# Optimization experiments

Measured on AMD Instinct MI355X. Metric: run time of the kernel, lower is better.

Reference implementation:

```python
import jax, jax.numpy as jnp
import numpy as np
from jax import lax

N_CLASS, SOS, EOS, NEG = 5, 0, 4, -10000.0


def _lstm_dir(x, Wih, Whh, bih, bhh, reverse):
    # x: (T, B, Din); PyTorch gate order i, f, g, o
    T, B, _ = x.shape
    Hd = Whh.shape[1]
    h0 = jnp.zeros((B, Hd), x.dtype)

    def step(carry, xt):
        h, c = carry
        g = xt @ Wih.T + h @ Whh.T + bih + bhh
        i, f, gg, o = jnp.split(g, 4, axis=-1)
        c = jax.nn.sigmoid(f) * c + jax.nn.sigmoid(i) * jnp.tanh(gg)
        h = jax.nn.sigmoid(o) * jnp.tanh(c)
        return (h, c), h

    xs = x[::-1] if reverse else x
    _, hs = lax.scan(step, (h0, h0), xs)
    return hs[::-1] if reverse else hs


def _forward(input_ids, tags, mask, emb, convs, lstm_params, lin_w, lin_b, transition):
    T, B = mask.shape
    x = emb[input_ids][:, None]  # (N, 1, L, E)
    pooled = []
    for w, b in convs:  # w: (K, 1, size, E)
        c = lax.conv_general_dilated(x, w, (1, 1), 'VALID',
                                     dimension_numbers=('NCHW', 'OIHW', 'NCHW'))
        c = jax.nn.relu(c[..., 0] + b[None, :, None])  # (N, K, L-size+1)
        pooled.append(jnp.max(c, axis=2))              # max-pool over length
    para = jnp.concatenate(pooled, axis=1)             # (N, 3K)
    h = para.reshape(B, T, -1).transpose(1, 0, 2)      # (T, B, 3K); equal para_len
    for (Wf, Uf, bf, cf, Wb, Ub, bb, cb) in lstm_params:  # 2-layer BiLSTM (eval: no dropout)
        hf = _lstm_dir(h, Wf, Uf, bf, cf, False)
        hb = _lstm_dir(h, Wb, Ub, bb, cb, True)
        h = jnp.concatenate([hf, hb], axis=-1)
    m = mask[..., None]
    feats = ((h * m) @ lin_w.T + lin_b) * m            # (T, B, 5)

    # CRF forward algorithm (log partition)
    alpha0 = jnp.full((B, N_CLASS), NEG, feats.dtype).at[:, SOS].set(0.0)

    def step(alpha, inp):
        feat, mt = inp
        s = alpha[:, None, :] + transition[None] + feat[:, :, None]
        new = jax.nn.logsumexp(s, axis=-1)
        return new * mt[:, None] + alpha * (1.0 - mt[:, None]), None

    alpha, _ = lax.scan(step, alpha0, (feats, mask))
    fwd_score = jax.nn.logsumexp(alpha + transition[EOS][None], axis=-1)

    # gold path score
    tags_ext = jnp.concatenate([jnp.full((1, B), SOS, tags.dtype), tags], 0)  # (T+1, B)
    emit = jnp.take_along_axis(feats, tags[..., None], axis=-1)[..., 0]       # (T, B)
    trans = transition[tags_ext[1:], tags_ext[:-1]]                           # (T, B)
    gold = jnp.sum((emit + trans) * mask, axis=0)
    lengths = mask.sum(0).astype(jnp.int32)
    last = tags_ext[lengths, jnp.arange(B)]
    gold = gold + transition[EOS, last]
    return (fwd_score - gold).sum()


def setup_inputs() -> dict:
    key = jax.random.key(0)
    ks = jax.random.split(key, 32)
    B, T, L, V, E, K, H = 8, 64, 64, 50000, 768, 256, 64
    N = B * T
    inp = {}
    inp['input_ids'] = jax.random.randint(ks[0], (N, L), 1, V)
    inp['tags'] = jax.random.randint(ks[1], (T, B), 1, 4)  # B/I/O tags
    inp['mask'] = jnp.ones((T, B), jnp.float32)
    inp['para_len'] = jnp.full((B,), T, jnp.int32)
    inp['emb'] = jax.random.normal(ks[2], (V, E)) * 0.1
    for i, sz in enumerate((3, 4, 5)):
        inp[f'cw{sz}'] = jax.random.normal(ks[3 + i], (K, 1, sz, E)) * (1.0 / np.sqrt(sz * E))
        inp[f'cb{sz}'] = jnp.zeros((K,), jnp.float32)
    kidx = 6
    for layer, din in ((0, 3 * K), (1, 2 * H)):
        for d in 'fb':
            inp[f'Wih{layer}{d}'] = jax.random.normal(ks[kidx], (4 * H, din)) * (1.0 / np.sqrt(din)); kidx += 1
            inp[f'Whh{layer}{d}'] = jax.random.normal(ks[kidx], (4 * H, H)) * (1.0 / np.sqrt(H)); kidx += 1
            inp[f'bih{layer}{d}'] = jnp.zeros((4 * H,), jnp.float32)
            inp[f'bhh{layer}{d}'] = jnp.zeros((4 * H,), jnp.float32)
    inp['lin_w'] = jax.random.normal(ks[kidx], (N_CLASS, 2 * H)) * 0.1; kidx += 1
    inp['lin_b'] = jnp.zeros((N_CLASS,), jnp.float32)
    tr = jax.random.normal(ks[kidx], (N_CLASS, N_CLASS))
    inp['transition'] = tr.at[SOS, :].set(NEG).at[:, EOS].set(NEG)
    return inp


def reference(input_ids, tags, mask, para_len, emb, cw3, cb3, cw4, cb4, cw5, cb5,
              Wih0f, Whh0f, bih0f, bhh0f, Wih0b, Whh0b, bih0b, bhh0b,
              Wih1f, Whh1f, bih1f, bhh1f, Wih1b, Whh1b, bih1b, bhh1b,
              lin_w, lin_b, transition):
    convs = ((cw3, cb3), (cw4, cb4), (cw5, cb5))
    lstm_params = ((Wih0f, Whh0f, bih0f, bhh0f, Wih0b, Whh0b, bih0b, bhh0b),
                   (Wih1f, Whh1f, bih1f, bhh1f, Wih1b, Whh1b, bih1b, bhh1b))
    return _forward(input_ids, tags, mask, emb, convs, lstm_params, lin_w, lin_b, transition)
```

## Files before the change

### kernel.cpp

```cpp
#include <hip/hip_runtime.h>
#include <cstdint>
#include <cstddef>

#define DEV __device__ __forceinline__

typedef __bf16 bf16x8 __attribute__((ext_vector_type(8)));
typedef float f32x4 __attribute__((ext_vector_type(4)));

#define NEG_VAL -10000.0f

DEV unsigned int f2bf(float f) {
    unsigned int u = __float_as_uint(f);
    return (u + 0x7FFFu + ((u >> 16) & 1u)) >> 16;
}
DEV unsigned int pk2(float a, float b) { return f2bf(a) | (f2bf(b) << 16); }

DEV float sigf(float x)  { return __builtin_amdgcn_rcpf(1.f + __expf(-x)); }
DEV float tanhff(float x){ return 2.f * __builtin_amdgcn_rcpf(1.f + __expf(-2.f * x)) - 1.f; }

__global__ void cast_all_kernel(const float* __restrict__ cw3,
                                const float* __restrict__ cw4,
                                const float* __restrict__ cw5,
                                const float* __restrict__ Wih0f,
                                const float* __restrict__ Wih0b,
                                const float* __restrict__ Wih1f,
                                const float* __restrict__ Wih1b,
                                unsigned short* __restrict__ wbc,
                                unsigned short* __restrict__ wih0c,
                                unsigned short* __restrict__ wih1c) {
    int tid = blockIdx.x * blockDim.x + threadIdx.x;
    const float* src;
    uint4* dstp;
    if (tid < 294912) {
        int g   = tid & 3;
        int col = (tid >> 2) & 255;
        int c   = (tid >> 10) % 24;
        int p   = tid / (24 * 256 * 4);
        int sz, j; const float* W;
        if (p < 3)      { sz = 3; j = p;     W = cw3; }
        else if (p < 7) { sz = 4; j = p - 3; W = cw4; }
        else            { sz = 5; j = p - 7; W = cw5; }
        src = W + ((size_t)col * sz + j) * 768 + c * 32 + g * 8;
        dstp = reinterpret_cast<uint4*>(wbc) +
               ((size_t)(p * 24 + c) * 1024 + (col >> 4) * 64 + g * 16 + (col & 15));
    } else if (tid < 294912 + 49152) {
        int u   = tid - 294912;
        int g   = u & 3;
        int col = (u >> 2) & 255;
        int kc  = (u >> 10) % 24;
        int dir = u / (24 * 256 * 4);
        const float* W = dir ? Wih0b : Wih0f;
        src = W + (size_t)col * 768 + kc * 32 + g * 8;
        dstp = reinterpret_cast<uint4*>(wih0c) +
               ((size_t)(dir * 24 + kc) * 1024 + (col >> 4) * 64 + g * 16 + (col & 15));
    } else if (tid < 294912 + 49152 + 8192) {
        int u   = tid - 294912 - 49152;
        int g   = u & 3;
        int col = (u >> 2) & 255;
        int kc  = (u >> 10) % 4;
        int dir = u / (4 * 256 * 4);
        const float* W = dir ? Wih1b : Wih1f;
        src = W + (size_t)col * 128 + kc * 32 + g * 8;
        dstp = reinterpret_cast<uint4*>(wih1c) +
               ((size_t)(dir * 4 + kc) * 1024 + (col >> 4) * 64 + g * 16 + (col & 15));
    } else return;
    float4 a = *(const float4*)(src);
    float4 b = *(const float4*)(src + 4);
    *dstp = make_uint4(pk2(a.x, a.y), pk2(a.z, a.w), pk2(b.x, b.y), pk2(b.z, b.w));
}

template<int SZ>
DEV void conv_body(const int* __restrict__ ids,
                   const float* __restrict__ emb,
                   const unsigned short* __restrict__ wbc,
                   const float* __restrict__ cb,
                   unsigned short* __restrict__ para_bf,
                   int pair, int szi, int pbase,
                   unsigned short* Xlds)
{
    int tid  = threadIdx.x;
    int lane = tid & 63;
    int nw   = tid >> 6;
    int l15  = lane & 15;
    int q    = lane >> 4;
    int n0   = pair * 2;

    int srow  = tid >> 1;
    int shalf = tid & 1;
    int sid   = ids[(n0 + (srow >> 6)) * 64 + (srow & 63)];
    const float* embrow = emb + (size_t)sid * 768 + shalf * 16;
    int skey = (srow >> 1) & 3;
    int xo0 = srow * 32 + (((2 * shalf)     ^ skey) * 8);
    int xo1 = srow * 32 + (((2 * shalf + 1) ^ skey) * 8);

    int vlaneB = nw * 2048 + lane * 8;

    f32x4 acc[8][4];
    #pragma unroll
    for (int a = 0; a < 8; a++)
        #pragma unroll
        for (int t = 0; t < 4; t++) acc[a][t] = (f32x4){0.f, 0.f, 0.f, 0.f};

    bf16x8 bfr[2][4];
    float4 e0, e1, e2, e3;

    {
        e0 = ((const float4*)embrow)[0];
        e1 = ((const float4*)embrow)[1];
        e2 = ((const float4*)embrow)[2];
        e3 = ((const float4*)embrow)[3];
        const unsigned short* bt = wbc + (size_t)(pbase * 24) * 8192 + vlaneB;
        #pragma unroll
        for (int t = 0; t < 4; t++)
            bfr[0][t] = *(const bf16x8*)(bt + t * 512);
        uint4 p0 = make_uint4(pk2(e0.x, e0.y), pk2(e0.z, e0.w),
                              pk2(e1.x, e1.y), pk2(e1.z, e1.w));
        uint4 p1 = make_uint4(pk2(e2.x, e2.y), pk2(e2.z, e2.w),
                              pk2(e3.x, e3.y), pk2(e3.z, e3.w));
        *(uint4*)&Xlds[xo0] = p0;
        *(uint4*)&Xlds[xo1] = p1;
        asm volatile("s_waitcnt lgkmcnt(0)" ::: "memory");
        __builtin_amdgcn_s_barrier();
    }

    int cbase = pbase * 24;
    for (int c2 = 0; c2 < 24; c2 += 2, cbase += 2) {
        #pragma unroll
        for (int s2 = 0; s2 < 2 * SZ; ++s2) {
            const int half = (s2 < SZ) ? 0 : 1;
            const int j    = s2 - half * SZ;
            const int par  = s2 & 1;
            {
                const int sP = s2 + 1;
                const int offP = (sP < SZ) ? sP * 24
                               : (sP < 2 * SZ ? (sP - SZ) * 24 + 1 : 2);
                const unsigned short* bt =
                    wbc + (size_t)(cbase + offP) * 8192 + vlaneB;
                #pragma unroll
                for (int t = 0; t < 4; t++)
                    bfr[par ^ 1][t] = *(const bf16x8*)(bt + t * 512);
            }
            if (s2 == 0 || s2 == SZ) {
                int cE = half ? c2 + 2 : c2 + 1; if (cE > 23) cE = 0;
                const float* sp = embrow + cE * 32;
                e0 = ((const float4*)sp)[0];
                e1 = ((const float4*)sp)[1];
                e2 = ((const float4*)sp)[2];
                e3 = ((const float4*)sp)[3];
            }

            const unsigned short* Xb = Xlds + half * 4096;
            {
                bf16x8 af[4];
                #pragma unroll
                for (int a = 0; a < 4; a++) {
                    int pp = 16 * a + l15 + j; if (pp > 63) pp = 63;
                    af[a] = *(const bf16x8*)(
                        &Xb[pp * 32 + ((q ^ ((pp >> 1) & 3)) * 8)]);
                }
                __builtin_amdgcn_s_setprio(1);
                #pragma unroll
                for (int a = 0; a < 4; a++)
                    #pragma unroll
                    for (int t = 0; t < 4; t++)
                        acc[a][t] = __builtin_amdgcn_mfma_f32_16x16x32_bf16(
                            af[a], bfr[par][t], acc[a][t], 0, 0, 0);
                __builtin_amdgcn_s_setprio(0);
            }
            {
                bf16x8 af[4];
                #pragma unroll
                for (int a = 0; a < 4; a++) {
                    int pp = 16 * a + l15 + j; if (pp > 63) pp = 63;
                    int xr = 64 + pp;
                    af[a] = *(const bf16x8*)(
                        &Xb[xr * 32 + ((q ^ ((xr >> 1) & 3)) * 8)]);
                }
                __builtin_amdgcn_s_setprio(1);
                #pragma unroll
                for (int a = 0; a < 4; a++)
                    #pragma unroll
                    for (int t = 0; t < 4; t++)
                        acc[4 + a][t] = __builtin_amdgcn_mfma_f32_16x16x32_bf16(
                            af[a], bfr[par][t], acc[4 + a][t], 0, 0, 0);
                __builtin_amdgcn_s_setprio(0);
            }

            if (j == SZ - 1) {
                unsigned short* Xw = Xlds + (half ^ 1) * 4096;
                uint4 p0 = make_uint4(pk2(e0.x, e0.y), pk2(e0.z, e0.w),
                                      pk2(e1.x, e1.y), pk2(e1.z, e1.w));
                uint4 p1 = make_uint4(pk2(e2.x, e2.y), pk2(e2.z, e2.w),
                                      pk2(e3.x, e3.y), pk2(e3.z, e3.w));
                *(uint4*)&Xw[xo0] = p0;
                *(uint4*)&Xw[xo1] = p1;
                asm volatile("s_waitcnt lgkmcnt(0)" ::: "memory");
                __builtin_amdgcn_s_barrier();
            }
        }
    }

    int pmax = 64 - SZ;
    #pragma unroll
    for (int t = 0; t < 4; t++) {
        int colb = nw * 64 + t * 16;
        float bias = cb[colb + l15];
        #pragma unroll
        for (int s = 0; s < 2; s++) {
            float m = 0.0f;
            #pragma unroll
            for (int a4 = 0; a4 < 4; a4++) {
                #pragma unroll
                for (int r = 0; r < 4; r++) {
                    int p = 16 * a4 + q * 4 + r;
                    float v = acc[s * 4 + a4][t][r] + bias;
                    v = v > 0.f ? v : 0.f;
                    if (p <= pmax) m = v > m ? v : m;
                }
            }
            m = fmaxf(m, __shfl_xor(m, 16));
            m = fmaxf(m, __shfl_xor(m, 32));
            if (lane < 16) {
                int n = n0 + s;
                int row = (n & 63) * 8 + (n >> 6);
                para_bf[(size_t)row * 768 + szi * 256 + colb + lane] =
                    (unsigned short)f2bf(m);
            }
        }
    }
}

__global__ __launch_bounds__(256, 2) void conv_pool_kernel(
    const int* __restrict__ ids,
    const float* __restrict__ emb,
    const unsigned short* __restrict__ wbc,
    const float* __restrict__ cb3, const float* __restrict__ cb4,
    const float* __restrict__ cb5,
    unsigned short* __restrict__ para_bf)
{
    __shared__ unsigned short Xlds[2][4096];
    int bx   = blockIdx.x;
    int szi  = 2 - (bx >> 8);
    int pair = bx & 255;
    if (szi == 0)
        conv_body<3>(ids, emb, wbc, cb3, para_bf, pair, 0, 0, &Xlds[0][0]);
    else if (szi == 1)
        conv_body<4>(ids, emb, wbc, cb4, para_bf, pair, 1, 3, &Xlds[0][0]);
    else
        conv_body<5>(ids, emb, wbc, cb5, para_bf, pair, 2, 7, &Xlds[0][0]);
}

template<int KC>
__global__ __launch_bounds__(256) void gemm_in_kernel(
    const unsigned short* __restrict__ xbf,
    const unsigned short* __restrict__ wihc,
    const float* __restrict__ bihF, const float* __restrict__ bhhF,
    const float* __restrict__ bihB, const float* __restrict__ bhhB,
    float* __restrict__ gates2)
{
    const int din = KC * 32;
    int bx   = blockIdx.x;
    int dir  = bx >> 4;
    int rowg = (bx >> 1) & 7;
    int colg = bx & 1;
    int tid  = threadIdx.x;
    int lane = tid & 63;
    int wid  = tid >> 6;
    int mw   = wid >> 1;
    int nw   = wid & 1;
    int l15  = lane & 15;
    int q    = lane >> 4;

    const float* bih = dir ? bihB : bihF;
    const float* bhh = dir ? bhhB : bhhF;
    const unsigned short* wt = wihc + (size_t)dir * KC * 8192;

    const unsigned short* arow[2];
    #pragma unroll
    for (int a = 0; a < 2; a++)
        arow[a] = xbf + (size_t)(rowg * 64 + mw * 32 + a * 16 + l15) * din + q * 8;
    const unsigned short* bbase = wt + (colg * 8 + nw * 4) * 512 + lane * 8;

    f32x4 acc[2][4];
    #pragma unroll
    for (int a = 0; a < 2; a++)
        #pragma unroll
        for (int t = 0; t < 4; t++) acc[a][t] = (f32x4){0.f, 0.f, 0.f, 0.f};

    bf16x8 afb[4][2], bfb[4][4];
    #pragma unroll
    for (int s = 0; s < 3; s++) {
        int k0 = (s < KC) ? s : KC - 1;
        #pragma unroll
        for (int a = 0; a < 2; a++)
            afb[s][a] = *(const bf16x8*)(arow[a] + k0 * 32);
        #pragma unroll
        for (int t = 0; t < 4; t++)
            bfb[s][t] = *(const bf16x8*)(bbase + (size_t)k0 * 8192 + t * 512);
    }

    #pragma unroll 4
    for (int kc = 0; kc < KC; ++kc) {
        const int p  = kc & 3;
        const int pn = (kc + 3) & 3;
        int kn = (kc + 3 < KC) ? kc + 3 : KC - 1;
        #pragma unroll
        for (int a = 0; a < 2; a++)
            afb[pn][a] = *(const bf16x8*)(arow[a] + kn * 32);
        #pragma unroll
        for (int t = 0; t < 4; t++)
            bfb[pn][t] = *(const bf16x8*)(bbase + (size_t)kn * 8192 + t * 512);
        #pragma unroll
        for (int a = 0; a < 2; a++)
            #pragma unroll
            for (int t = 0; t < 4; t++)
                acc[a][t] = __builtin_amdgcn_mfma_f32_16x16x32_bf16(
                    afb[p][a], bfb[p][t], acc[a][t], 0, 0, 0);
    }

    #pragma unroll
    for (int tt = 0; tt < 4; tt++) {
        int nn = colg * 128 + nw * 64 + tt * 16 + l15;
        float bb = bih[nn] + bhh[nn];
        #pragma unroll
        for (int a = 0; a < 2; a++) {
            int m = rowg * 64 + mw * 32 + q * 4 + a * 16;
            int tcol = m >> 3, b0 = m & 7;
            f32x4 v = acc[a][tt];
            v[0] += bb; v[1] += bb; v[2] += bb; v[3] += bb;
            *(f32x4*)(gates2 + (((size_t)dir * 64 + tcol) * 256 + nn) * 8 + b0) = v;
        }
    }
}

__global__ __launch_bounds__(256) void lstm_rec_kernel(
    const float* __restrict__ gates2,
    const float* __restrict__ WhhF, const float* __restrict__ WhhB,
    float* __restrict__ houtF,
    unsigned short* __restrict__ houtB)
{
    int dir = blockIdx.x;
    const float* Whh = dir ? WhhB : WhhF;
    const float* gin = gates2 + (size_t)dir * 64 * 256 * 8;

    __shared__ unsigned short h16[2][16 * 64];

    int tid  = threadIdx.x;
    int lane = tid & 63;
    int w    = tid >> 6;
    int l15  = lane & 15;
    int q    = lane >> 4;
    int hh   = 16 * w + l15;

    bf16x8 Bf[4][2];
    #pragma unroll
    for (int g = 0; g < 4; g++)
        #pragma unroll
        for (int kh = 0; kh < 2; kh++) {
            const float* wp = Whh + (size_t)(g * 64 + hh) * 64 + kh * 32 + q * 8;
            float4 f0 = *(const float4*)wp;
            float4 f1 = *(const float4*)(wp + 4);
            bf16x8 r;
            r[0] = (__bf16)f0.x; r[1] = (__bf16)f0.y;
            r[2] = (__bf16)f0.z; r[3] = (__bf16)f0.w;
            r[4] = (__bf16)f1.x; r[5] = (__bf16)f1.y;
            r[6] = (__bf16)f1.z; r[7] = (__bf16)f1.w;
            Bf[g][kh] = r;
        }

    const float* pgB[4];
    #pragma unroll
    for (int g = 0; g < 4; g++)
        pgB[g] = gin + (size_t)(g * 64 + hh) * 8 + 4 * q;

    for (int i = tid; i < 2 * 16 * 64; i += 256)
        ((unsigned short*)h16)[i] = 0;
    float cst[4] = {0.f, 0.f, 0.f, 0.f};
    __syncthreads();

    f32x4 gvp[4][4];
    #pragma unroll
    for (int d = 0; d < 3; d++) {
        int td = dir ? 63 - d : d;
        #pragma unroll
        for (int g = 0; g < 4; g++)
            gvp[d][g] = *(const f32x4*)(pgB[g] + (size_t)td * 2048);
    }

    #pragma unroll 4
    for (int s = 0; s < 64; ++s) {
        const int slot = s & 3;
        int t = dir ? 63 - s : s;
        const unsigned short* hb = h16[s & 1];
        int slot0 = q ^ (l15 & 7);
        int slot1 = (4 + q) ^ (l15 & 7);
        bf16x8 a0 = *(const bf16x8*)&hb[l15 * 64 + slot0 * 8];
        bf16x8 a1 = *(const bf16x8*)&hb[l15 * 64 + slot1 * 8];

        f32x4 acc[4];
        #pragma unroll
        for (int g = 0; g < 4; g++) {
            acc[g] = __builtin_amdgcn_mfma_f32_16x16x32_bf16(a0, Bf[g][0], gvp[slot][g], 0, 0, 0);
            acc[g] = __builtin_amdgcn_mfma_f32_16x16x32_bf16(a1, Bf[g][1], acc[g], 0, 0, 0);
        }

        {
            int sn = (s + 3 < 64) ? s + 3 : 63;
            int tn = dir ? 63 - sn : sn;
            const int slotn = (s + 3) & 3;
            #pragma unroll
            for (int g = 0; g < 4; g++)
                gvp[slotn][g] = *(const f32x4*)(pgB[g] + (size_t)tn * 2048);
        }

        if (q < 2) {
            unsigned short* hw = h16[(s + 1) & 1];
            #pragma unroll
            for (int r = 0; r < 4; r++) {
                int b = 4 * q + r;
                float gi = acc[0][r];
                float gf = acc[1][r];
                float gg = acc[2][r];
                float go = acc[3][r];
                float cn = sigf(gf) * cst[r] + sigf(gi) * tanhff(gg);
                float hv = sigf(go) * tanhff(cn);
                cst[r] = cn;
                int slotw = (hh >> 3) ^ (b & 7);
                hw[b * 64 + slotw * 8 + (hh & 7)] = (unsigned short)f2bf(hv);
                size_t oi = ((size_t)t * 8 + b) * 128 + dir * 64 + hh;
                if (houtF) houtF[oi] = hv;
                houtB[oi] = (unsigned short)f2bf(hv);
            }
        }
        __syncthreads();
    }
}

__global__ __launch_bounds__(512) void crf_kernel(
    const float* __restrict__ h1,
    const float* __restrict__ lin_w,
    const float* __restrict__ lin_b,
    const float* __restrict__ mask,
    const int* __restrict__ tags,
    const float* __restrict__ trans,
    float* __restrict__ out) {
    __shared__ float feats[64][8][5];
    __shared__ float wl[5][128];
    __shared__ float msk[512];
    __shared__ int   tgs[512];
    __shared__ float fwd_s[8], gold_s[8];
    __shared__ float tr[25], trE[5], lb[5];
    int tid = threadIdx.x;
    if (tid < 25) tr[tid] = trans[tid];
    if (tid < 5) { trE[tid] = trans[20 + tid]; lb[tid] = lin_b[tid]; }
    msk[tid] = mask[tid];
    tgs[tid] = tags[tid];
    if (tid < 128) {
        #pragma unroll
        for (int i = 0; i < 5; i++) wl[i][tid] = lin_w[i * 128 + tid];
    }
    __syncthreads();

    {
        const float4* h4 = (const float4*)(h1 + (size_t)tid * 128);
        float a0 = 0.f, a1 = 0.f, a2 = 0.f, a3 = 0.f, a4 = 0.f;
        for (int e4 = 0; e4 < 32; e4++) {
            float4 hv = h4[e4];
            int e = e4 * 4;
            a0 += hv.x * wl[0][e] + hv.y * wl[0][e+1] + hv.z * wl[0][e+2] + hv.w * wl[0][e+3];
            a1 += hv.x * wl[1][e] + hv.y * wl[1][e+1] + hv.z * wl[1][e+2] + hv.w * wl[1][e+3];
            a2 += hv.x * wl[2][e] + hv.y * wl[2][e+1] + hv.z * wl[2][e+2] + hv.w * wl[2][e+3];
            a3 += hv.x * wl[3][e] + hv.y * wl[3][e+1] + hv.z * wl[3][e+2] + hv.w * wl[3][e+3];
            a4 += hv.x * wl[4][e] + hv.y * wl[4][e+1] + hv.z * wl[4][e+2] + hv.w * wl[4][e+3];
        }
        float m = msk[tid];
        int t = tid >> 3, b = tid & 7;
        feats[t][b][0] = (m * a0 + lb[0]) * m;
        feats[t][b][1] = (m * a1 + lb[1]) * m;
        feats[t][b][2] = (m * a2 + lb[2]) * m;
        feats[t][b][3] = (m * a3 + lb[3]) * m;
        feats[t][b][4] = (m * a4 + lb[4]) * m;
    }
    __syncthreads();

    if (tid < 40) {
        int b = tid / 5, i = tid % 5;
        float alpha = (i == 0) ? 0.f : NEG_VAL;
        float trow[5];
        #pragma unroll
        for (int j2 = 0; j2 < 5; j2++) trow[j2] = tr[i * 5 + j2];
        for (int t = 0; t < 64; t++) {
            float s0, s1, s2, s3, s4;
            s0 = __shfl(alpha, b * 5 + 0, 64) + trow[0];
            s1 = __shfl(alpha, b * 5 + 1, 64) + trow[1];
            s2 = __shfl(alpha, b * 5 + 2, 64) + trow[2];
            s3 = __shfl(alpha, b * 5 + 3, 64) + trow[3];
            s4 = __shfl(alpha, b * 5 + 4, 64) + trow[4];
            float mx = fmaxf(fmaxf(fmaxf(s0, s1), fmaxf(s2, s3)), s4);
            float sum = expf(s0 - mx) + expf(s1 - mx) + expf(s2 - mx) +
                        expf(s3 - mx) + expf(s4 - mx);
            float lse = mx + logf(sum) + feats[t][b][i];
            float mt = msk[t * 8 + b];
            alpha = mt * lse + (1.f - mt) * alpha;
        }
        float v = alpha + trE[i];
        float m0 = __shfl(v, b * 5 + 0, 64);
        float m1 = __shfl(v, b * 5 + 1, 64);
        float m2 = __shfl(v, b * 5 + 2, 64);
        float m3 = __shfl(v, b * 5 + 3, 64);
        float m4 = __shfl(v, b * 5 + 4, 64);
        float mx = fmaxf(fmaxf(fmaxf(m0, m1), fmaxf(m2, m3)), m4);
        float sum = expf(m0 - mx) + expf(m1 - mx) + expf(m2 - mx) +
                    expf(m3 - mx) + expf(m4 - mx);
        if (i == 0) fwd_s[b] = mx + logf(sum);
    }
    if (tid >= 64 && tid < 72) {
        int b = tid - 64;
        float g = 0.f, lenf = 0.f;
        int prev = 0;
        for (int t = 0; t < 64; t++) {
            int tg = tgs[t * 8 + b];
            float mt = msk[t * 8 + b];
            g += (feats[t][b][tg] + tr[tg * 5 + prev]) * mt;
            lenf += mt;
            prev = tg;
        }
        int len = (int)lenf;
        int last = (len == 0) ? 0 : tgs[(len - 1) * 8 + b];
        g += trE[last];
        gold_s[b] = g;
    }
    __syncthreads();
    if (tid == 0) {
        float s = 0.f;
        for (int b = 0; b < 8; b++) s += fwd_s[b] - gold_s[b];
        out[0] = s;
    }
}

extern "C" void kernel_launch(void* const* d_in, const int* in_sizes, int n_in,
                              void* d_out, int out_size, void* d_ws, size_t ws_size,
                              hipStream_t stream) {
    const int*   ids   = (const int*)d_in[0];
    const int*   tags  = (const int*)d_in[1];
    const float* mask  = (const float*)d_in[2];
    const float* emb   = (const float*)d_in[4];
    const float* cw3   = (const float*)d_in[5];
    const float* cb3   = (const float*)d_in[6];
    const float* cw4   = (const float*)d_in[7];
    const float* cb4   = (const float*)d_in[8];
    const float* cw5   = (const float*)d_in[9];
    const float* cb5   = (const float*)d_in[10];
    const float* Wih0f = (const float*)d_in[11];
    const float* Whh0f = (const float*)d_in[12];
    const float* bih0f = (const float*)d_in[13];
    const float* bhh0f = (const float*)d_in[14];
    const float* Wih0b = (const float*)d_in[15];
    const float* Whh0b = (const float*)d_in[16];
    const float* bih0b = (const float*)d_in[17];
    const float* bhh0b = (const float*)d_in[18];
    const float* Wih1f = (const float*)d_in[19];
    const float* Whh1f = (const float*)d_in[20];
    const float* bih1f = (const float*)d_in[21];
    const float* bhh1f = (const float*)d_in[22];
    const float* Wih1b = (const float*)d_in[23];
    const float* Whh1b = (const float*)d_in[24];
    const float* bih1b = (const float*)d_in[25];
    const float* bhh1b = (const float*)d_in[26];
    const float* lin_w = (const float*)d_in[27];
    const float* lin_b = (const float*)d_in[28];
    const float* trans = (const float*)d_in[29];

    char* ws = (char*)d_ws;
    unsigned short* wbc     = (unsigned short*)ws;
    unsigned short* wih0c   = (unsigned short*)(ws + 4718592);
    unsigned short* wih1c   = (unsigned short*)(ws + 5505024);
    unsigned short* para_bf = (unsigned short*)(ws + 5636096);
    float*          gates   = (float*)(ws + 6422528);
    unsigned short* h0_bf   = (unsigned short*)(ws + 5636096);
    float*          h1f     = (float*)(ws + 4718592);

    hipLaunchKernelGGL(cast_all_kernel, dim3(1376), dim3(256), 0, stream,
                       cw3, cw4, cw5, Wih0f, Wih0b, Wih1f, Wih1b,
                       wbc, wih0c, wih1c);
    hipLaunchKernelGGL(conv_pool_kernel, dim3(768), dim3(256), 0, stream,
                       ids, emb, wbc, cb3, cb4, cb5, para_bf);
    hipLaunchKernelGGL((gemm_in_kernel<24>), dim3(32), dim3(256), 0, stream,
                       para_bf, wih0c, bih0f, bhh0f, bih0b, bhh0b, gates);
    hipLaunchKernelGGL(lstm_rec_kernel, dim3(2), dim3(256), 0, stream,
                       gates, Whh0f, Whh0b, (float*)nullptr, h0_bf);
    hipLaunchKernelGGL((gemm_in_kernel<4>), dim3(32), dim3(256), 0, stream,
                       h0_bf, wih1c, bih1f, bhh1f, bih1b, bhh1b, gates);
    hipLaunchKernelGGL(lstm_rec_kernel, dim3(2), dim3(256), 0, stream,
                       gates, Whh1f, Whh1b, h1f, h0_bf);
    hipLaunchKernelGGL(crf_kernel, dim3(1), dim3(512), 0, stream,
                       h1f, lin_w, lin_b, mask, tags, trans, (float*)d_out);
}
```

Before: 250.3 us.

## Fuse GEMM, LSTM recurrence and CRF stages into one cooperative kernel

```diff
diff --git a/kernel.cpp b/kernel.cpp
--- a/kernel.cpp
+++ b/kernel.cpp
@@ -1,6 +1,9 @@
 #include <hip/hip_runtime.h>
+#include <hip/hip_cooperative_groups.h>
 #include <cstdint>
 #include <cstddef>
+
+namespace cg = cooperative_groups;
 
 #define DEV __device__ __forceinline__
 
@@ -250,16 +253,30 @@
         conv_body<5>(ids, emb, wbc, cb5, para_bf, pair, 2, 7, &Xlds[0][0]);
 }
 
+struct TailArgs {
+    const unsigned short* para_bf;
+    const unsigned short* wih0c;
+    const unsigned short* wih1c;
+    const float *bih0f, *bhh0f, *bih0b, *bhh0b;
+    const float *bih1f, *bhh1f, *bih1b, *bhh1b;
+    const float *Whh0f, *Whh0b, *Whh1f, *Whh1b;
+    float* gates;
+    unsigned short* h0_bf;
+    float* h1f;
+    const float* lin_w; const float* lin_b;
+    const float* mask; const int* tags; const float* trans;
+    float* out;
+};
+
 template<int KC>
-__global__ __launch_bounds__(256) void gemm_in_kernel(
-    const unsigned short* __restrict__ xbf,
-    const unsigned short* __restrict__ wihc,
-    const float* __restrict__ bihF, const float* __restrict__ bhhF,
-    const float* __restrict__ bihB, const float* __restrict__ bhhB,
-    float* __restrict__ gates2)
+DEV void gemm_phase(int bx,
+                    const unsigned short* __restrict__ xbf,
+                    const unsigned short* __restrict__ wihc,
+                    const float* bihF, const float* bhhF,
+                    const float* bihB, const float* bhhB,
+                    float* __restrict__ gates2)
 {
     const int din = KC * 32;
-    int bx   = blockIdx.x;
     int dir  = bx >> 4;
     int rowg = (bx >> 1) & 7;
     int colg = bx & 1;
@@ -333,17 +350,15 @@
     }
 }
 
-__global__ __launch_bounds__(256) void lstm_rec_kernel(
-    const float* __restrict__ gates2,
-    const float* __restrict__ WhhF, const float* __restrict__ WhhB,
-    float* __restrict__ houtF,
-    unsigned short* __restrict__ houtB)
+DEV void lstm_phase(char* smemraw, int dir,
+                    const float* __restrict__ gates2,
+                    const float* __restrict__ Whh,
+                    float* __restrict__ houtF,
+                    unsigned short* __restrict__ houtB)
 {
-    int dir = blockIdx.x;
-    const float* Whh = dir ? WhhB : WhhF;
+    unsigned short (*h16)[16 * 64] =
+        reinterpret_cast<unsigned short (*)[16 * 64]>(smemraw);
     const float* gin = gates2 + (size_t)dir * 64 * 256 * 8;
-
-    __shared__ unsigned short h16[2][16 * 64];
 
     int tid  = threadIdx.x;
     int lane = tid & 63;
@@ -436,50 +451,57 @@
     }
 }
 
-__global__ __launch_bounds__(512) void crf_kernel(
-    const float* __restrict__ h1,
-    const float* __restrict__ lin_w,
-    const float* __restrict__ lin_b,
-    const float* __restrict__ mask,
-    const int* __restrict__ tags,
-    const float* __restrict__ trans,
-    float* __restrict__ out) {
-    __shared__ float feats[64][8][5];
-    __shared__ float wl[5][128];
-    __shared__ float msk[512];
-    __shared__ int   tgs[512];
-    __shared__ float fwd_s[8], gold_s[8];
-    __shared__ float tr[25], trE[5], lb[5];
+struct CrfSmem {
+    float feats[64][8][5];
+    float wl[5][128];
+    float msk[512];
+    int   tgs[512];
+    float fwd_s[8], gold_s[8];
+    float tr[25], trE[5], lb[5];
+};
+
+DEV void crf_phase(char* smemraw,
+                   const float* __restrict__ h1,
+                   const float* __restrict__ lin_w,
+                   const float* __restrict__ lin_b,
+                   const float* __restrict__ mask,
+                   const int* __restrict__ tags,
+                   const float* __restrict__ trans,
+                   float* __restrict__ out)
+{
+    CrfSmem& S = *reinterpret_cast<CrfSmem*>(smemraw);
     int tid = threadIdx.x;
-    if (tid < 25) tr[tid] = trans[tid];
-    if (tid < 5) { trE[tid] = trans[20 + tid]; lb[tid] = lin_b[tid]; }
-    msk[tid] = mask[tid];
-    tgs[tid] = tags[tid];
+    if (tid < 25) S.tr[tid] = trans[tid];
+    if (tid < 5) { S.trE[tid] = trans[20 + tid]; S.lb[tid] = lin_b[tid]; }
+    for (int i = tid; i < 512; i += 256) {
+        S.msk[i] = mask[i];
+        S.tgs[i] = tags[i];
+    }
     if (tid < 128) {
         #pragma unroll
-        for (int i = 0; i < 5; i++) wl[i][tid] = lin_w[i * 128 + tid];
+        for (int i = 0; i < 5; i++) S.wl[i][tid] = lin_w[i * 128 + tid];
     }
     __syncthreads();
 
-    {
-        const float4* h4 = (const float4*)(h1 + (size_t)tid * 128);
+    for (int rr = tid; rr < 512; rr += 256) {
+        const float4* h4 = (const float4*)(h1 + (size_t)rr * 128);
         float a0 = 0.f, a1 = 0.f, a2 = 0.f, a3 = 0.f, a4 = 0.f;
         for (int e4 = 0; e4 < 32; e4++) {
             float4 hv = h4[e4];
             int e = e4 * 4;
-            a0 += hv.x * wl[0][e] + hv.y * wl[0][e+1] + hv.z * wl[0][e+2] + hv.w * wl[0][e+3];
-            a1 += hv.x * wl[1][e] + hv.y * wl[1][e+1] + hv.z * wl[1][e+2] + hv.w * wl[1][e+3];
-            a2 += hv.x * wl[2][e] + hv.y * wl[2][e+1] + hv.z * wl[2][e+2] + hv.w * wl[2][e+3];
-            a3 += hv.x * wl[3][e] + hv.y * wl[3][e+1] + hv.z * wl[3][e+2] + hv.w * wl[3][e+3];
-            a4 += hv.x * wl[4][e] + hv.y * wl[4][e+1] + hv.z * wl[4][e+2] + hv.w * wl[4][e+3];
-        }
-        float m = msk[tid];
-        int t = tid >> 3, b = tid & 7;
-        feats[t][b][0] = (m * a0 + lb[0]) * m;
-        feats[t][b][1] = (m * a1 + lb[1]) * m;
-        feats[t][b][2] = (m * a2 + lb[2]) * m;
-        feats[t][b][3] = (m * a3 + lb[3]) * m;
-        feats[t][b][4] = (m * a4 + lb[4]) * m;
+            a0 += hv.x * S.wl[0][e] + hv.y * S.wl[0][e+1] + hv.z * S.wl[0][e+2] + hv.w * S.wl[0][e+3];
+            a1 += hv.x * S.wl[1][e] + hv.y * S.wl[1][e+1] + hv.z * S.wl[1][e+2] + hv.w * S.wl[1][e+3];
+            a2 += hv.x * S.wl[2][e] + hv.y * S.wl[2][e+1] + hv.z * S.wl[2][e+2] + hv.w * S.wl[2][e+3];
+            a3 += hv.x * S.wl[3][e] + hv.y * S.wl[3][e+1] + hv.z * S.wl[3][e+2] + hv.w * S.wl[3][e+3];
+            a4 += hv.x * S.wl[4][e] + hv.y * S.wl[4][e+1] + hv.z * S.wl[4][e+2] + hv.w * S.wl[4][e+3];
+        }
+        float m = S.msk[rr];
+        int t = rr >> 3, b = rr & 7;
+        S.feats[t][b][0] = (m * a0 + S.lb[0]) * m;
+        S.feats[t][b][1] = (m * a1 + S.lb[1]) * m;
+        S.feats[t][b][2] = (m * a2 + S.lb[2]) * m;
+        S.feats[t][b][3] = (m * a3 + S.lb[3]) * m;
+        S.feats[t][b][4] = (m * a4 + S.lb[4]) * m;
     }
     __syncthreads();
 
@@ -488,7 +510,7 @@
         float alpha = (i == 0) ? 0.f : NEG_VAL;
         float trow[5];
         #pragma unroll
-        for (int j2 = 0; j2 < 5; j2++) trow[j2] = tr[i * 5 + j2];
+        for (int j2 = 0; j2 < 5; j2++) trow[j2] = S.tr[i * 5 + j2];
         for (int t = 0; t < 64; t++) {
             float s0, s1, s2, s3, s4;
             s0 = __shfl(alpha, b * 5 + 0, 64) + trow[0];
@@ -499,11 +521,11 @@
             float mx = fmaxf(fmaxf(fmaxf(s0, s1), fmaxf(s2, s3)), s4);
             float sum = expf(s0 - mx) + expf(s1 - mx) + expf(s2 - mx) +
                         expf(s3 - mx) + expf(s4 - mx);
-            float lse = mx + logf(sum) + feats[t][b][i];
-            float mt = msk[t * 8 + b];
+            float lse = mx + logf(sum) + S.feats[t][b][i];
+            float mt = S.msk[t * 8 + b];
             alpha = mt * lse + (1.f - mt) * alpha;
         }
-        float v = alpha + trE[i];
+        float v = alpha + S.trE[i];
         float m0 = __shfl(v, b * 5 + 0, 64);
         float m1 = __shfl(v, b * 5 + 1, 64);
         float m2 = __shfl(v, b * 5 + 2, 64);
@@ -512,30 +534,55 @@
         float mx = fmaxf(fmaxf(fmaxf(m0, m1), fmaxf(m2, m3)), m4);
         float sum = expf(m0 - mx) + expf(m1 - mx) + expf(m2 - mx) +
                     expf(m3 - mx) + expf(m4 - mx);
-        if (i == 0) fwd_s[b] = mx + logf(sum);
+        if (i == 0) S.fwd_s[b] = mx + logf(sum);
     }
     if (tid >= 64 && tid < 72) {
         int b = tid - 64;
         float g = 0.f, lenf = 0.f;
         int prev = 0;
         for (int t = 0; t < 64; t++) {
-            int tg = tgs[t * 8 + b];
-            float mt = msk[t * 8 + b];
-            g += (feats[t][b][tg] + tr[tg * 5 + prev]) * mt;
+            int tg = S.tgs[t * 8 + b];
+            float mt = S.msk[t * 8 + b];
+            g += (S.feats[t][b][tg] + S.tr[tg * 5 + prev]) * mt;
             lenf += mt;
             prev = tg;
         }
         int len = (int)lenf;
-        int last = (len == 0) ? 0 : tgs[(len - 1) * 8 + b];
-        g += trE[last];
-        gold_s[b] = g;
+        int last = (len == 0) ? 0 : S.tgs[(len - 1) * 8 + b];
+        g += S.trE[last];
+        S.gold_s[b] = g;
     }
     __syncthreads();
     if (tid == 0) {
         float s = 0.f;
-        for (int b = 0; b < 8; b++) s += fwd_s[b] - gold_s[b];
+        for (int b = 0; b < 8; b++) s += S.fwd_s[b] - S.gold_s[b];
         out[0] = s;
     }
+}
+
+__global__ __launch_bounds__(256) void tail_kernel(TailArgs a)
+{
+    cg::grid_group grid = cg::this_grid();
+    __shared__ __align__(16) char smem[sizeof(CrfSmem)];
+    int bx = blockIdx.x;
+
+    gemm_phase<24>(bx, a.para_bf, a.wih0c, a.bih0f, a.bhh0f, a.bih0b, a.bhh0b,
+                   a.gates);
+    grid.sync();
+    if (bx < 2)
+        lstm_phase(smem, bx, a.gates, bx ? a.Whh0b : a.Whh0f,
+                   (float*)nullptr, a.h0_bf);
+    grid.sync();
+    gemm_phase<4>(bx, a.h0_bf, a.wih1c, a.bih1f, a.bhh1f, a.bih1b, a.bhh1b,
+                  a.gates);
+    grid.sync();
+    if (bx < 2)
+        lstm_phase(smem, bx, a.gates, bx ? a.Whh1b : a.Whh1f,
+                   a.h1f, a.h0_bf);
+    grid.sync();
+    if (bx == 0)
+        crf_phase(smem, a.h1f, a.lin_w, a.lin_b, a.mask, a.tags, a.trans,
+                  a.out);
 }
 
 extern "C" void kernel_launch(void* const* d_in, const int* in_sizes, int n_in,
@@ -585,14 +632,18 @@
                        wbc, wih0c, wih1c);
     hipLaunchKernelGGL(conv_pool_kernel, dim3(768), dim3(256), 0, stream,
                        ids, emb, wbc, cb3, cb4, cb5, para_bf);
-    hipLaunchKernelGGL((gemm_in_kernel<24>), dim3(32), dim3(256), 0, stream,
-                       para_bf, wih0c, bih0f, bhh0f, bih0b, bhh0b, gates);
-    hipLaunchKernelGGL(lstm_rec_kernel, dim3(2), dim3(256), 0, stream,
-                       gates, Whh0f, Whh0b, (float*)nullptr, h0_bf);
-    hipLaunchKernelGGL((gemm_in_kernel<4>), dim3(32), dim3(256), 0, stream,
-                       h0_bf, wih1c, bih1f, bhh1f, bih1b, bhh1b, gates);
-    hipLaunchKernelGGL(lstm_rec_kernel, dim3(2), dim3(256), 0, stream,
-                       gates, Whh1f, Whh1b, h1f, h0_bf);
-    hipLaunchKernelGGL(crf_kernel, dim3(1), dim3(512), 0, stream,
-                       h1f, lin_w, lin_b, mask, tags, trans, (float*)d_out);
-}
+
+    TailArgs ta;
+    ta.para_bf = para_bf;
+    ta.wih0c = wih0c; ta.wih1c = wih1c;
+    ta.bih0f = bih0f; ta.bhh0f = bhh0f; ta.bih0b = bih0b; ta.bhh0b = bhh0b;
+    ta.bih1f = bih1f; ta.bhh1f = bhh1f; ta.bih1b = bih1b; ta.bhh1b = bhh1b;
+    ta.Whh0f = Whh0f; ta.Whh0b = Whh0b; ta.Whh1f = Whh1f; ta.Whh1b = Whh1b;
+    ta.gates = gates; ta.h0_bf = h0_bf; ta.h1f = h1f;
+    ta.lin_w = lin_w; ta.lin_b = lin_b;
+    ta.mask = mask; ta.tags = tags; ta.trans = trans;
+    ta.out = (float*)d_out;
+    void* args[] = { &ta };
+    hipLaunchCooperativeKernel(reinterpret_cast<void*>(tail_kernel),
+                               dim3(32), dim3(256), args, 0, stream);
+}
```

New measurement: 278.2 us. 1.11x slower.
